# Kernel tuning notes

Measured on AMD Instinct MI355X. Metric: run time of the kernel, lower is better.

The kernel has to match this reference:

```python
import jax, jax.numpy as jnp
import numpy as np

IN_FEATURES = 256
OUT_FEATURES = 64
ALPHA = 0.2  # leaky relu slope


def _xavier_uniform(key, shape, gain=1.414):
    fan_in, fan_out = shape[0], shape[1]
    limit = gain * np.sqrt(6.0 / (fan_in + fan_out))
    return jax.random.uniform(key, shape, jnp.float32, -limit, limit)


def setup_inputs() -> dict:
    key = jax.random.key(0)
    k_h, k_W, k_a = jax.random.split(key, 3)
    h = jax.random.normal(k_h, (8, 2048, IN_FEATURES), dtype=jnp.float32)
    W = _xavier_uniform(k_W, (IN_FEATURES, OUT_FEATURES))
    a = _xavier_uniform(k_a, (2 * OUT_FEATURES, 1))
    return {"h": h, "W": W, "a": a}


def reference(h, W, a):
    # h: [B, N, F_in], W: [F_in, D], a: [2D, 1]
    Wh = h @ W  # [B, N, D]
    D = Wh.shape[-1]
    a1 = a[:D, 0]   # attends to source node i (repeat_interleave side)
    a2 = a[D:, 0]   # attends to target node j (repeat side)
    f1 = Wh @ a1    # [B, N]
    f2 = Wh @ a2    # [B, N]
    # e[b, i, j] = leakyrelu(a1.Wh[b,i] + a2.Wh[b,j])  -- identical math to
    # the original's O(N^2 * 2D) repeat/concat, without materializing it.
    e = jax.nn.leaky_relu(f1[:, :, None] + f2[:, None, :], negative_slope=ALPHA)  # [B, N, N]
    # NOTE: original applies softmax over dim=1 (over i, per column j).
    attention = jax.nn.softmax(e, axis=1)  # [B, N, N]
    # dropout is identity in eval mode
    h_prime = jnp.einsum('bij,bjd->bid', attention, Wh)  # [B, N, D]
    return jax.nn.elu(h_prime)  # concat=True path
```

## Files before the change

### kernel.cpp

```cpp
#include <hip/hip_runtime.h>

#define B 8
#define N 2048
#define KF 256
#define DF 64
#define LOG2E 1.44269504088896340736f
#define IC 8
#define ICH (N / IC)

typedef __attribute__((ext_vector_type(8))) short short8;
typedef __attribute__((ext_vector_type(4))) float float4v;

__device__ __forceinline__ float fexp2(float x) {
#if __has_builtin(__builtin_amdgcn_exp2f)
    return __builtin_amdgcn_exp2f(x);
#else
    return exp2f(x);
#endif
}
__device__ __forceinline__ float eluf(float x) {
    return x > 0.f ? x : fexp2(x * LOG2E) - 1.0f;
}
__device__ __forceinline__ short bf16r(float x) {
    unsigned u = __float_as_uint(x);
    return (short)((u + 0x8000u) >> 16);
}
#define DOT4(c, u, p) \
    p = fmaf(c.x, u.x, fmaf(c.y, u.y, fmaf(c.z, u.z, fmaf(c.w, u.w, p))));

__global__ __launch_bounds__(256) void k_wh(const float* __restrict__ h,
                                            const float* __restrict__ W,
                                            const float* __restrict__ a,
                                            short* __restrict__ WhT,
                                            float* __restrict__ f1,
                                            float* __restrict__ f2) {
    __shared__ __align__(16) unsigned char smem[34816];
    short* lwt  = (short*)smem;
    float* lv   = (float*)(smem + 32768);
    float* lred = (float*)smem;
    float* lp   = (float*)(smem + 16896);

    int t = threadIdx.x;
    int wv = t >> 6, lane = t & 63;
    int n15 = lane & 15, q = lane >> 4;
    int bx = blockIdx.x;

    const float* hr = h + ((long)bx * 32 + n15) * KF + wv * 64 + q * 8;
    float4 c0 = *(const float4*)(hr);
    float4 c1 = *(const float4*)(hr + 4);
    float4 c2 = *(const float4*)(hr + 32);
    float4 c3 = *(const float4*)(hr + 36);

    {
        const float4* wr4 = (const float4*)(W + t * DF);
        float s1 = 0.f, s2 = 0.f;
        #pragma unroll
        for (int c = 0; c < 16; c++) {
            float4 w4 = wr4[c];
            float4 a1v = *(const float4*)(a + 4 * c);
            float4 a2v = *(const float4*)(a + DF + 4 * c);
            lwt[(4 * c + 0) * 256 + t] = bf16r(w4.x);
            lwt[(4 * c + 1) * 256 + t] = bf16r(w4.y);
            lwt[(4 * c + 2) * 256 + t] = bf16r(w4.z);
            lwt[(4 * c + 3) * 256 + t] = bf16r(w4.w);
            s1 = fmaf(w4.x, a1v.x, fmaf(w4.y, a1v.y, fmaf(w4.z, a1v.z, fmaf(w4.w, a1v.w, s1))));
            s2 = fmaf(w4.x, a2v.x, fmaf(w4.y, a2v.y, fmaf(w4.z, a2v.z, fmaf(w4.w, a2v.w, s2))));
        }
        lv[t] = s1;
        lv[256 + t] = s2;
    }
    __syncthreads();

    const short* bq = lwt + n15 * 256 + wv * 64 + q * 8;
    short8 s0b0 = *(const short8*)(bq);
    short8 s0b1 = *(const short8*)(bq + 16 * 256);
    short8 s0b2 = *(const short8*)(bq + 32 * 256);
    short8 s0b3 = *(const short8*)(bq + 48 * 256);
    short8 s1b0 = *(const short8*)(bq + 32);
    short8 s1b1 = *(const short8*)(bq + 16 * 256 + 32);
    short8 s1b2 = *(const short8*)(bq + 32 * 256 + 32);
    short8 s1b3 = *(const short8*)(bq + 48 * 256 + 32);
    const float* vv = lv + wv * 64 + q * 8;
    float4 u00 = *(const float4*)(vv);
    float4 u01 = *(const float4*)(vv + 4);
    float4 u10 = *(const float4*)(vv + 32);
    float4 u11 = *(const float4*)(vv + 36);
    float4 x00 = *(const float4*)(vv + 256);
    float4 x01 = *(const float4*)(vv + 256 + 4);
    float4 x10 = *(const float4*)(vv + 256 + 32);
    float4 x11 = *(const float4*)(vv + 256 + 36);
    __syncthreads();

    #pragma unroll
    for (int rt = 0; rt < 2; rt++) {
        float4 m0, m1, m2, m3;
        if (rt < 1) {
            const float* hn = hr + 16 * KF;
            m0 = *(const float4*)(hn);
            m1 = *(const float4*)(hn + 4);
            m2 = *(const float4*)(hn + 32);
            m3 = *(const float4*)(hn + 36);
        }
        float p1 = 0.f, p2 = 0.f;
        DOT4(c0, u00, p1) DOT4(c1, u01, p1) DOT4(c2, u10, p1) DOT4(c3, u11, p1)
        DOT4(c0, x00, p2) DOT4(c1, x01, p2) DOT4(c2, x10, p2) DOT4(c3, x11, p2)

        short8 af0 = { bf16r(c0.x), bf16r(c0.y), bf16r(c0.z), bf16r(c0.w),
                       bf16r(c1.x), bf16r(c1.y), bf16r(c1.z), bf16r(c1.w) };
        short8 af1 = { bf16r(c2.x), bf16r(c2.y), bf16r(c2.z), bf16r(c2.w),
                       bf16r(c3.x), bf16r(c3.y), bf16r(c3.z), bf16r(c3.w) };
        float4v acc0 = {0.f, 0.f, 0.f, 0.f}, acc1 = acc0, acc2 = acc0, acc3 = acc0;
        acc0 = __builtin_amdgcn_mfma_f32_16x16x32_bf16(af0, s0b0, acc0, 0, 0, 0);
        acc0 = __builtin_amdgcn_mfma_f32_16x16x32_bf16(af1, s1b0, acc0, 0, 0, 0);
        acc1 = __builtin_amdgcn_mfma_f32_16x16x32_bf16(af0, s0b1, acc1, 0, 0, 0);
        acc1 = __builtin_amdgcn_mfma_f32_16x16x32_bf16(af1, s1b1, acc1, 0, 0, 0);
        acc2 = __builtin_amdgcn_mfma_f32_16x16x32_bf16(af0, s0b2, acc2, 0, 0, 0);
        acc2 = __builtin_amdgcn_mfma_f32_16x16x32_bf16(af1, s1b2, acc2, 0, 0, 0);
        acc3 = __builtin_amdgcn_mfma_f32_16x16x32_bf16(af0, s0b3, acc3, 0, 0, 0);
        acc3 = __builtin_amdgcn_mfma_f32_16x16x32_bf16(af1, s1b3, acc3, 0, 0, 0);

        #define STASH(nb, A)                                                  \
            {                                                                 \
                _Pragma("unroll")                                             \
                for (int r = 0; r < 4; r++)                                   \
                    lred[wv * 1056 + (q * 4 + r) * 66 + nb * 16 + n15] = A[r]; \
            }
        STASH(0, acc0) STASH(1, acc1) STASH(2, acc2) STASH(3, acc3)
        #undef STASH
        p1 += __shfl_xor(p1, 16, 64); p1 += __shfl_xor(p1, 32, 64);
        p2 += __shfl_xor(p2, 16, 64); p2 += __shfl_xor(p2, 32, 64);
        if (q == 0) { lp[wv * 16 + n15] = p1; lp[64 + wv * 16 + n15] = p2; }
        __syncthreads();

        long i0 = (long)bx * 32 + rt * 16;
        int d = t & 63, ig = t >> 6;
        int bb = (int)(i0 >> 11);
        int il = (int)(i0 & (N - 1));
        float s0 = 0.f, s1 = 0.f, s2 = 0.f, s3 = 0.f;
        #pragma unroll
        for (int w = 0; w < 4; w++) {
            const float* lr = lred + w * 1056 + (ig * 4) * 66 + d;
            s0 += lr[0]; s1 += lr[66]; s2 += lr[132]; s3 += lr[198];
        }
        short4 pk = make_short4(bf16r(s0), bf16r(s1), bf16r(s2), bf16r(s3));
        int jj = il + ig * 4;
        *(short4*)(WhT + (((long)bb * 32 + (jj >> 6)) * 64 + d) * 64 + (jj & 63)) = pk;

        if (t < 16) {
            f1[i0 + t] = lp[t] + lp[16 + t] + lp[32 + t] + lp[48 + t];
        } else if (t < 32) {
            int tt = t + 48;
            f2[i0 + t - 16] = lp[tt] + lp[16 + tt] + lp[32 + tt] + lp[48 + tt];
        }
        __syncthreads();
        c0 = m0; c1 = m1; c2 = m2; c3 = m3;
    }
}

__global__ __launch_bounds__(256) void k_denom(const float* __restrict__ f1,
                                               const float* __restrict__ f2,
                                               float* __restrict__ dpart) {
    __shared__ float2 le[ICH];
    int t = threadIdx.x;
    int b = blockIdx.z, ic = blockIdx.y;
    int j = blockIdx.x * 256 + t;
    float v = f1[b * N + ic * ICH + t];
    le[t] = make_float2(fexp2(v * LOG2E), fexp2(v * 0.2f * LOG2E));
    __syncthreads();
    float f2j = f2[b * N + j];
    float E2  = fexp2(f2j * LOG2E);
    float E2s = fexp2(f2j * 0.2f * LOG2E);
    float s = 0.f;
    const float4* le4 = (const float4*)le;
    for (int ii = 0; ii < ICH / 2; ii++) {
        float4 u = le4[ii];
        s += fmaxf(u.x * E2, u.y * E2s);
        s += fmaxf(u.z * E2, u.w * E2s);
    }
    dpart[((long)ic * B + b) * N + j] = s;
}

__global__ __launch_bounds__(512) void k_attn(const short* __restrict__ WhT,
                                              const float* __restrict__ f1,
                                              const float* __restrict__ f2,
                                              const float* __restrict__ dpart,
                                              float* __restrict__ out) {
    __shared__ __align__(16) unsigned char smem[40960];
    int t = threadIdx.x;
    int wv = t >> 6, lane = t & 63;
    int g = wv >> 1, wg = wv & 1, lt2 = t & 127;
    int n15 = lane & 15, q = lane >> 4;
    int it = blockIdx.x, b = blockIdx.y;
    int i0 = it * 64 + wg * 32;

    float f1a = f1[b * N + i0 + n15];
    float f1b = f1[b * N + i0 + 16 + n15];
    float E1a = fexp2(f1a * LOG2E),  E1sa = fexp2(f1a * 0.2f * LOG2E);
    float E1b = fexp2(f1b * LOG2E),  E1sb = fexp2(f1b * 0.2f * LOG2E);

    uint4*  ls = (uint4*)smem + g * 576;
    float2* lc = (float2*)(smem + 36864) + g * 128;
    const uint4* wsrc = (const uint4*)WhT + ((long)b * 32 + g * 8) * 512;
    const float* f2b = f2 + b * N + g * 512;
    const float* dpb = dpart + b * N + g * 512;

    uint4 r0, r1, r2, r3;
    float pf2, pd0, pd1, pd2, pd3, pd4, pd5, pd6, pd7;

    #define LOADC(cc) {                                     \
        const uint4* gp = wsrc + (cc) * 512;                \
        r0 = gp[lt2];       r1 = gp[128 + lt2];             \
        r2 = gp[256 + lt2]; r3 = gp[384 + lt2];             \
    }
    #define LOADP(cc) {                                     \
        if (lt2 < 64) {                                     \
            int jb2 = (cc) * 64 + lt2;                      \
            pf2 = f2b[jb2];                                 \
            pd0 = dpb[jb2];              pd1 = dpb[16384 + jb2]; \
            pd2 = dpb[2 * 16384 + jb2];  pd3 = dpb[3 * 16384 + jb2]; \
            pd4 = dpb[4 * 16384 + jb2];  pd5 = dpb[5 * 16384 + jb2]; \
            pd6 = dpb[6 * 16384 + jb2];  pd7 = dpb[7 * 16384 + jb2]; \
        }                                                   \
    }
    #define STOREC() {                                      \
        int rb = lt2 >> 3, cl = lt2 & 7;                    \
        ls[rb * 9 + cl] = r0;        ls[(16 + rb) * 9 + cl] = r1; \
        ls[(32 + rb) * 9 + cl] = r2; ls[(48 + rb) * 9 + cl] = r3; \
    }
    #define LCC(buf) {                                      \
        if (lt2 < 64) {                                     \
            float den = ((pd0 + pd1) + (pd2 + pd3)) + ((pd4 + pd5) + (pd6 + pd7)); \
            float rr = 1.0f / den;                          \
            float E2  = fexp2(pf2 * LOG2E);                 \
            float E2s = fexp2(pf2 * 0.2f * LOG2E);          \
            lc[(buf) * 64 + lt2] = make_float2(E2 * rr, E2s * rr); \
        }                                                   \
    }

    LOADC(0) LOADP(0)
    STOREC() LCC(0)
    __syncthreads();

    float4v accA0 = {0.f, 0.f, 0.f, 0.f}, accA1 = accA0, accA2 = accA0, accA3 = accA0;
    float4v accB0 = accA0, accB1 = accA0, accB2 = accA0, accB3 = accA0;

    for (int c = 0; c < 8; c++) {
        int cur = c & 1;
        if (c < 7) { LOADC(c + 1) LOADP(c + 1) }

        const short* lsS = (const short*)ls;
        const float4* lcf = (const float4*)(lc + cur * 64);
        #pragma unroll
        for (int js = 0; js < 2; js++) {
            const float4* cp4 = lcf + js * 16 + q * 4;
            float4 p01 = cp4[0], p23 = cp4[1], p45 = cp4[2], p67 = cp4[3];
            short8 afA, afB;
            #define PE(px, py, DI) {                                  \
                afA[DI] = bf16r(fmaxf(E1a * (px), E1sa * (py)));      \
                afB[DI] = bf16r(fmaxf(E1b * (px), E1sb * (py)));      \
            }
            PE(p01.x, p01.y, 0) PE(p01.z, p01.w, 1)
            PE(p23.x, p23.y, 2) PE(p23.z, p23.w, 3)
            PE(p45.x, p45.y, 4) PE(p45.z, p45.w, 5)
            PE(p67.x, p67.y, 6) PE(p67.z, p67.w, 7)
            #undef PE

            const short* bp = lsS + js * 32 + q * 8;
            short8 b0 = *(const short8*)(bp + (n15 +  0) * 72);
            short8 b1 = *(const short8*)(bp + (n15 + 16) * 72);
            short8 b2 = *(const short8*)(bp + (n15 + 32) * 72);
            short8 b3 = *(const short8*)(bp + (n15 + 48) * 72);

            accA0 = __builtin_amdgcn_mfma_f32_16x16x32_bf16(afA, b0, accA0, 0, 0, 0);
            accA1 = __builtin_amdgcn_mfma_f32_16x16x32_bf16(afA, b1, accA1, 0, 0, 0);
            accA2 = __builtin_amdgcn_mfma_f32_16x16x32_bf16(afA, b2, accA2, 0, 0, 0);
            accA3 = __builtin_amdgcn_mfma_f32_16x16x32_bf16(afA, b3, accA3, 0, 0, 0);
            accB0 = __builtin_amdgcn_mfma_f32_16x16x32_bf16(afB, b0, accB0, 0, 0, 0);
            accB1 = __builtin_amdgcn_mfma_f32_16x16x32_bf16(afB, b1, accB1, 0, 0, 0);
            accB2 = __builtin_amdgcn_mfma_f32_16x16x32_bf16(afB, b2, accB2, 0, 0, 0);
            accB3 = __builtin_amdgcn_mfma_f32_16x16x32_bf16(afB, b3, accB3, 0, 0, 0);
        }

        if (c < 7) {
            __syncthreads();
            STOREC() LCC((c + 1) & 1)
            __syncthreads();
        }
    }
    #undef LOADC
    #undef LOADP
    #undef STOREC
    #undef LCC

    float* epi = (float*)smem;
    int row_o = t >> 3, d0 = (t & 7) * 8;
    int wg_o = row_o >> 5, r31 = row_o & 31;
    const float* e1p = epi + wg_o * 2176 + r31 * 68 + d0;
    const float* e2p = epi + (2 + wg_o) * 2176 + r31 * 68 + d0;

    #define ESTASH(rg) {                                                     \
        float* ep = epi + (rg) * 2176 + (q * 4) * 68 + n15;                  \
        _Pragma("unroll")                                                    \
        for (int r = 0; r < 4; r++) {                                        \
            ep[r * 68 +  0] = accA0[r]; ep[r * 68 + 16] = accA1[r];          \
            ep[r * 68 + 32] = accA2[r]; ep[r * 68 + 48] = accA3[r];          \
            ep[(16 * 68) + r * 68 +  0] = accB0[r];                          \
            ep[(16 * 68) + r * 68 + 16] = accB1[r];                          \
            ep[(16 * 68) + r * 68 + 32] = accB2[r];                          \
            ep[(16 * 68) + r * 68 + 48] = accB3[r];                          \
        }                                                                    \
    }

    __syncthreads();
    if (g < 2) ESTASH(wv)
    __syncthreads();
    float4 sa0 = *(const float4*)(e1p);
    float4 sa1 = *(const float4*)(e1p + 4);
    float4 sb0 = *(const float4*)(e2p);
    float4 sb1 = *(const float4*)(e2p + 4);
    float4 t0, t1;
    t0.x = sa0.x + sb0.x; t0.y = sa0.y + sb0.y; t0.z = sa0.z + sb0.z; t0.w = sa0.w + sb0.w;
    t1.x = sa1.x + sb1.x; t1.y = sa1.y + sb1.y; t1.z = sa1.z + sb1.z; t1.w = sa1.w + sb1.w;
    __syncthreads();
    if (g >= 2) ESTASH(wv - 4)
    __syncthreads();
    #undef ESTASH
    float4 ua0 = *(const float4*)(e1p);
    float4 ua1 = *(const float4*)(e1p + 4);
    float4 ub0 = *(const float4*)(e2p);
    float4 ub1 = *(const float4*)(e2p + 4);
    float4 o0, o1;
    o0.x = eluf(t0.x + ua0.x + ub0.x); o0.y = eluf(t0.y + ua0.y + ub0.y);
    o0.z = eluf(t0.z + ua0.z + ub0.z); o0.w = eluf(t0.w + ua0.w + ub0.w);
    o1.x = eluf(t1.x + ua1.x + ub1.x); o1.y = eluf(t1.y + ua1.y + ub1.y);
    o1.z = eluf(t1.z + ua1.z + ub1.z); o1.w = eluf(t1.w + ua1.w + ub1.w);
    float* op = out + ((long)b * N + it * 64 + row_o) * DF + d0;
    *(float4*)(op) = o0;
    *(float4*)(op + 4) = o1;
}

extern "C" void kernel_launch(void* const* d_in, const int* in_sizes, int n_in,
                              void* d_out, int out_size, void* d_ws, size_t ws_size,
                              hipStream_t stream) {
    const float* h = (const float*)d_in[0];
    const float* W = (const float*)d_in[1];
    const float* a = (const float*)d_in[2];
    float* out = (float*)d_out;

    char* ws = (char*)d_ws;
    const size_t NB = (size_t)B * N;
    size_t off = 0;
    short* WhT   = (short*)(ws + off); off += NB * DF * sizeof(short);
    float* f1    = (float*)(ws + off); off += NB * sizeof(float);
    float* f2    = (float*)(ws + off); off += NB * sizeof(float);
    float* dpart = (float*)(ws + off); off += (size_t)IC * NB * sizeof(float);
    (void)off; (void)ws_size;

    k_wh<<<NB / 32, 256, 0, stream>>>(h, W, a, WhT, f1, f2);
    k_denom<<<dim3(N / 256, IC, B), 256, 0, stream>>>(f1, f2, dpart);
    k_attn<<<dim3(N / 64, B), 512, 0, stream>>>(WhT, f1, f2, dpart, out);
}
```

Measured before the change: 91.75 us.

## Load WhT MFMA operands directly from global, drop LDS staging and loop syncs

Changes the WhT layout to plain [B, D, N] and has each lane read its MFMA B-operand fragments straight from global memory with a one-step register prefetch, instead of staging 64-column chunks through LDS. The per-column softmax scale factors for the whole 512-column group are computed once up front into LDS, which removes the per-chunk double barriers. The aim is to cut LDS traffic and synchronisation. In exchange it issues more, less coalesced global/L2 loads (16-byte strided per lane), and latency is hidden by only one iteration of prefetch.

```diff
diff --git a/kernel.cpp b/kernel.cpp
--- a/kernel.cpp
+++ b/kernel.cpp
@@ -144,7 +144,7 @@
         }
         short4 pk = make_short4(bf16r(s0), bf16r(s1), bf16r(s2), bf16r(s3));
         int jj = il + ig * 4;
-        *(short4*)(WhT + (((long)bb * 32 + (jj >> 6)) * 64 + d) * 64 + (jj & 63)) = pk;
+        *(short4*)(WhT + ((long)bb * DF + d) * N + jj) = pk;
 
         if (t < 16) {
             f1[i0 + t] = lp[t] + lp[16 + t] + lp[32 + t] + lp[48 + t];
@@ -185,7 +185,7 @@
                                               const float* __restrict__ f2,
                                               const float* __restrict__ dpart,
                                               float* __restrict__ out) {
-    __shared__ __align__(16) unsigned char smem[40960];
+    __shared__ __align__(16) unsigned char smem[34816];
     int t = threadIdx.x;
     int wv = t >> 6, lane = t & 63;
     int g = wv >> 1, wg = wv & 1, lt2 = t & 127;
@@ -198,99 +198,63 @@
     float E1a = fexp2(f1a * LOG2E),  E1sa = fexp2(f1a * 0.2f * LOG2E);
     float E1b = fexp2(f1b * LOG2E),  E1sb = fexp2(f1b * 0.2f * LOG2E);
 
-    uint4*  ls = (uint4*)smem + g * 576;
-    float2* lc = (float2*)(smem + 36864) + g * 128;
-    const uint4* wsrc = (const uint4*)WhT + ((long)b * 32 + g * 8) * 512;
+    float2* lc = (float2*)smem + g * 512;
     const float* f2b = f2 + b * N + g * 512;
     const float* dpb = dpart + b * N + g * 512;
 
-    uint4 r0, r1, r2, r3;
-    float pf2, pd0, pd1, pd2, pd3, pd4, pd5, pd6, pd7;
-
-    #define LOADC(cc) {                                     \
-        const uint4* gp = wsrc + (cc) * 512;                \
-        r0 = gp[lt2];       r1 = gp[128 + lt2];             \
-        r2 = gp[256 + lt2]; r3 = gp[384 + lt2];             \
-    }
-    #define LOADP(cc) {                                     \
-        if (lt2 < 64) {                                     \
-            int jb2 = (cc) * 64 + lt2;                      \
-            pf2 = f2b[jb2];                                 \
-            pd0 = dpb[jb2];              pd1 = dpb[16384 + jb2]; \
-            pd2 = dpb[2 * 16384 + jb2];  pd3 = dpb[3 * 16384 + jb2]; \
-            pd4 = dpb[4 * 16384 + jb2];  pd5 = dpb[5 * 16384 + jb2]; \
-            pd6 = dpb[6 * 16384 + jb2];  pd7 = dpb[7 * 16384 + jb2]; \
-        }                                                   \
-    }
-    #define STOREC() {                                      \
-        int rb = lt2 >> 3, cl = lt2 & 7;                    \
-        ls[rb * 9 + cl] = r0;        ls[(16 + rb) * 9 + cl] = r1; \
-        ls[(32 + rb) * 9 + cl] = r2; ls[(48 + rb) * 9 + cl] = r3; \
-    }
-    #define LCC(buf) {                                      \
-        if (lt2 < 64) {                                     \
-            float den = ((pd0 + pd1) + (pd2 + pd3)) + ((pd4 + pd5) + (pd6 + pd7)); \
-            float rr = 1.0f / den;                          \
-            float E2  = fexp2(pf2 * LOG2E);                 \
-            float E2s = fexp2(pf2 * 0.2f * LOG2E);          \
-            lc[(buf) * 64 + lt2] = make_float2(E2 * rr, E2s * rr); \
-        }                                                   \
-    }
-
-    LOADC(0) LOADP(0)
-    STOREC() LCC(0)
-    __syncthreads();
+    #pragma unroll
+    for (int s = 0; s < 4; s++) {
+        int j = s * 128 + lt2;
+        float pf2 = f2b[j];
+        float den = ((dpb[j] + dpb[16384 + j]) + (dpb[2 * 16384 + j] + dpb[3 * 16384 + j]))
+                  + ((dpb[4 * 16384 + j] + dpb[5 * 16384 + j]) + (dpb[6 * 16384 + j] + dpb[7 * 16384 + j]));
+        float rr = 1.0f / den;
+        lc[j] = make_float2(fexp2(pf2 * LOG2E) * rr, fexp2(pf2 * 0.2f * LOG2E) * rr);
+    }
+    __syncthreads();
+
+    const short* wb = WhT + (long)b * DF * N + (long)n15 * N + g * 512;
+    short8 nb0 = *(const short8*)(wb + q * 8);
+    short8 nb1 = *(const short8*)(wb + 16 * N + q * 8);
+    short8 nb2 = *(const short8*)(wb + 32 * N + q * 8);
+    short8 nb3 = *(const short8*)(wb + 48 * N + q * 8);
 
     float4v accA0 = {0.f, 0.f, 0.f, 0.f}, accA1 = accA0, accA2 = accA0, accA3 = accA0;
     float4v accB0 = accA0, accB1 = accA0, accB2 = accA0, accB3 = accA0;
 
-    for (int c = 0; c < 8; c++) {
-        int cur = c & 1;
-        if (c < 7) { LOADC(c + 1) LOADP(c + 1) }
-
-        const short* lsS = (const short*)ls;
-        const float4* lcf = (const float4*)(lc + cur * 64);
-        #pragma unroll
-        for (int js = 0; js < 2; js++) {
-            const float4* cp4 = lcf + js * 16 + q * 4;
-            float4 p01 = cp4[0], p23 = cp4[1], p45 = cp4[2], p67 = cp4[3];
-            short8 afA, afB;
-            #define PE(px, py, DI) {                                  \
-                afA[DI] = bf16r(fmaxf(E1a * (px), E1sa * (py)));      \
-                afB[DI] = bf16r(fmaxf(E1b * (px), E1sb * (py)));      \
-            }
-            PE(p01.x, p01.y, 0) PE(p01.z, p01.w, 1)
-            PE(p23.x, p23.y, 2) PE(p23.z, p23.w, 3)
-            PE(p45.x, p45.y, 4) PE(p45.z, p45.w, 5)
-            PE(p67.x, p67.y, 6) PE(p67.z, p67.w, 7)
-            #undef PE
-
-            const short* bp = lsS + js * 32 + q * 8;
-            short8 b0 = *(const short8*)(bp + (n15 +  0) * 72);
-            short8 b1 = *(const short8*)(bp + (n15 + 16) * 72);
-            short8 b2 = *(const short8*)(bp + (n15 + 32) * 72);
-            short8 b3 = *(const short8*)(bp + (n15 + 48) * 72);
-
-            accA0 = __builtin_amdgcn_mfma_f32_16x16x32_bf16(afA, b0, accA0, 0, 0, 0);
-            accA1 = __builtin_amdgcn_mfma_f32_16x16x32_bf16(afA, b1, accA1, 0, 0, 0);
-            accA2 = __builtin_amdgcn_mfma_f32_16x16x32_bf16(afA, b2, accA2, 0, 0, 0);
-            accA3 = __builtin_amdgcn_mfma_f32_16x16x32_bf16(afA, b3, accA3, 0, 0, 0);
-            accB0 = __builtin_amdgcn_mfma_f32_16x16x32_bf16(afB, b0, accB0, 0, 0, 0);
-            accB1 = __builtin_amdgcn_mfma_f32_16x16x32_bf16(afB, b1, accB1, 0, 0, 0);
-            accB2 = __builtin_amdgcn_mfma_f32_16x16x32_bf16(afB, b2, accB2, 0, 0, 0);
-            accB3 = __builtin_amdgcn_mfma_f32_16x16x32_bf16(afB, b3, accB3, 0, 0, 0);
-        }
-
-        if (c < 7) {
-            __syncthreads();
-            STOREC() LCC((c + 1) & 1)
-            __syncthreads();
-        }
-    }
-    #undef LOADC
-    #undef LOADP
-    #undef STOREC
-    #undef LCC
+    #pragma unroll 4
+    for (int js = 0; js < 16; js++) {
+        short8 b0 = nb0, b1 = nb1, b2 = nb2, b3 = nb3;
+        if (js < 15) {
+            const short* bp = wb + (js + 1) * 32 + q * 8;
+            nb0 = *(const short8*)(bp);
+            nb1 = *(const short8*)(bp + 16 * N);
+            nb2 = *(const short8*)(bp + 32 * N);
+            nb3 = *(const short8*)(bp + 48 * N);
+        }
+
+        const float4* cp4 = (const float4*)(lc + js * 32 + q * 8);
+        float4 p01 = cp4[0], p23 = cp4[1], p45 = cp4[2], p67 = cp4[3];
+        short8 afA, afB;
+        #define PE(px, py, DI) {                                  \
+            afA[DI] = bf16r(fmaxf(E1a * (px), E1sa * (py)));      \
+            afB[DI] = bf16r(fmaxf(E1b * (px), E1sb * (py)));      \
+        }
+        PE(p01.x, p01.y, 0) PE(p01.z, p01.w, 1)
+        PE(p23.x, p23.y, 2) PE(p23.z, p23.w, 3)
+        PE(p45.x, p45.y, 4) PE(p45.z, p45.w, 5)
+        PE(p67.x, p67.y, 6) PE(p67.z, p67.w, 7)
+        #undef PE
+
+        accA0 = __builtin_amdgcn_mfma_f32_16x16x32_bf16(afA, b0, accA0, 0, 0, 0);
+        accA1 = __builtin_amdgcn_mfma_f32_16x16x32_bf16(afA, b1, accA1, 0, 0, 0);
+        accA2 = __builtin_amdgcn_mfma_f32_16x16x32_bf16(afA, b2, accA2, 0, 0, 0);
+        accA3 = __builtin_amdgcn_mfma_f32_16x16x32_bf16(afA, b3, accA3, 0, 0, 0);
+        accB0 = __builtin_amdgcn_mfma_f32_16x16x32_bf16(afB, b0, accB0, 0, 0, 0);
+        accB1 = __builtin_amdgcn_mfma_f32_16x16x32_bf16(afB, b1, accB1, 0, 0, 0);
+        accB2 = __builtin_amdgcn_mfma_f32_16x16x32_bf16(afB, b2, accB2, 0, 0, 0);
+        accB3 = __builtin_amdgcn_mfma_f32_16x16x32_bf16(afB, b3, accB3, 0, 0, 0);
+    }
 
     float* epi = (float*)smem;
     int row_o = t >> 3, d0 = (t & 7) * 8;
```

Measured after the change: 98.52 us. 1.07x slower.
